# Optimization experiments

Hardware: AMD Instinct MI355X
Metric: run time of the kernel (lower is better)

## Reference

```python
import jax, jax.numpy as jnp
import numpy as np

WS = 8        # window size
NH = 8        # num heads


def setup_inputs() -> dict:
    key = jax.random.key(0)
    ks = jax.random.split(key, 6)
    B, C, H, W = 8, 256, 64, 64
    Cr = C // 4
    s = lambda n: 1.0 / np.sqrt(n)
    return {
        "x": jax.random.normal(ks[0], (B, C, H, W), jnp.float32),
        "ca_w1": jax.random.normal(ks[1], (Cr, C), jnp.float32) * s(C),
        "ca_b1": jnp.zeros((Cr,), jnp.float32),
        "ca_w2": jax.random.normal(ks[2], (C, Cr), jnp.float32) * s(Cr),
        "ca_b2": jnp.zeros((C,), jnp.float32),
        "in_proj_w": jax.random.normal(ks[3], (3 * C, C), jnp.float32) * s(C),
        "in_proj_b": jnp.zeros((3 * C,), jnp.float32),
        "out_proj_w": jax.random.normal(ks[4], (C, C), jnp.float32) * s(C),
        "out_proj_b": jnp.zeros((C,), jnp.float32),
    }


def reference(x, ca_w1, ca_b1, ca_w2, ca_b2, in_proj_w, in_proj_b, out_proj_w, out_proj_b):
    B, C, H, W = x.shape
    # ---- channel SE gate: AdaptiveAvgPool2d(1) -> 1x1 conv == linear ----
    pooled = x.mean(axis=(2, 3))                                   # [B, C]
    h1 = jax.nn.relu(pooled @ ca_w1.T + ca_b1)                     # [B, C/4]
    ca = jax.nn.sigmoid(h1 @ ca_w2.T + ca_b2)                      # [B, C]
    x = x * ca[:, :, None, None]

    # ---- window partition (non-overlapping unfold) ----
    Hw, Ww = H // WS, W // WS
    nwin = Hw * Ww
    xw = x.reshape(B, C, Hw, WS, Ww, WS).transpose(0, 1, 2, 4, 3, 5)   # [B,C,Hw,Ww,ws,ws]
    # view(B,C,nwin,ws*ws).permute(2,0,3,1).reshape(nwin*B, ws*ws, C)
    xw = xw.reshape(B, C, nwin, WS * WS).transpose(2, 0, 3, 1).reshape(nwin * B, WS * WS, C)

    # ---- nn.MultiheadAttention with batch_first=False: (L, N, E) ----
    # L = nwin*B (sequence!), N = ws*ws (batch!), E = C  -- faithful to source quirk
    L, N, _ = xw.shape
    hd = C // NH
    qkv = xw @ in_proj_w.T + in_proj_b                             # [L, N, 3C]
    q, k, v = jnp.split(qkv, 3, axis=-1)
    to_heads = lambda t: t.reshape(L, N, NH, hd).transpose(1, 2, 0, 3)  # [N, NH, L, hd]
    q, k, v = to_heads(q), to_heads(k), to_heads(v)
    scale = 1.0 / jnp.sqrt(jnp.asarray(hd, x.dtype))
    attn = jax.nn.softmax(jnp.einsum("nhld,nhmd->nhlm", q * scale, k), axis=-1)
    o = jnp.einsum("nhlm,nhmd->nhld", attn, v)                     # [N, NH, L, hd]
    o = o.transpose(2, 0, 1, 3).reshape(L, N, C)
    o = o @ out_proj_w.T + out_proj_b                              # [L, N, C]

    # ---- reshape back; nearest interpolate H*W -> H*W is identity ----
    o = o.reshape(nwin, B, WS * WS, C).transpose(1, 3, 0, 2)       # [B, C, nwin, ws*ws]
    x_out = o.reshape(B, C, H, W)
    return x + x_out
```

## Files before the change

kernel.cpp:

```cpp
#include <hip/hip_runtime.h>
#include <hip/hip_bf16.h>
#include <math.h>


typedef unsigned short ushort_t;
typedef unsigned int uint_t;
typedef __attribute__((ext_vector_type(8))) short bf16x8;
typedef __attribute__((ext_vector_type(4))) float f32x4;

#define ALPHA 0.25503486f

__device__ __forceinline__ uint_t pk_rne(float a, float b) {
    __hip_bfloat16 ha = __float2bfloat16(a), hb = __float2bfloat16(b);
    ushort_t ua = *(ushort_t*)&ha, ub = *(ushort_t*)&hb;
    return (uint_t)ua | ((uint_t)ub << 16);
}

__device__ __forceinline__ uint_t pk2(float a, float b) {
    union { float f; uint_t u; } ua, ub; ua.f = a; ub.f = b;
    return __builtin_amdgcn_perm(ua.u, ub.u, 0x03020706u);
}

__device__ __forceinline__ void gl_lds16(const ushort_t* g, ushort_t* l) {
    __builtin_amdgcn_global_load_lds(
        (__attribute__((address_space(1))) unsigned int*)(g),
        (__attribute__((address_space(3))) unsigned int*)(l), 16, 0, 0);
}

__global__ __launch_bounds__(256) void k_pre(const float* __restrict__ x,
                                             float* __restrict__ pooled,
                                             const float* __restrict__ ipw,
                                             ushort_t* __restrict__ Wqb,
                                             const float* __restrict__ opw,
                                             ushort_t* __restrict__ Wob) {
    int bx = blockIdx.x;
    int t = threadIdx.x;
    if (bx < 2048) {
        const float4* row4 = (const float4*)(x + (size_t)bx * 4096);
        float s = 0.f;
        for (int i = t; i < 1024; i += 256) {
            float4 v = row4[i];
            s += v.x + v.y + v.z + v.w;
        }
        __shared__ float red[256];
        red[t] = s;
        __syncthreads();
        for (int o = 128; o > 0; o >>= 1) {
            if (t < o) red[t] += red[t + o];
            __syncthreads();
        }
        if (t == 0) pooled[bx] = red[0] * (1.f / 4096.f);
    } else if (bx < 2144) {
        int i = (bx - 2048) * 256 + t;
        float sc = (i < 8192) ? ALPHA : 1.f;
        const float4* s4 = (const float4*)ipw + (size_t)i * 2;
        float4 a = s4[0], b = s4[1];
        uint4 u;
        u.x = pk_rne(a.x * sc, a.y * sc); u.y = pk_rne(a.z * sc, a.w * sc);
        u.z = pk_rne(b.x * sc, b.y * sc); u.w = pk_rne(b.z * sc, b.w * sc);
        *(uint4*)(Wqb + (size_t)i * 8) = u;
    } else {
        int i = (bx - 2144) * 256 + t;
        const float4* s4 = (const float4*)opw + (size_t)i * 2;
        float4 a = s4[0], b = s4[1];
        uint4 u;
        u.x = pk_rne(a.x, a.y); u.y = pk_rne(a.z, a.w);
        u.z = pk_rne(b.x, b.y); u.w = pk_rne(b.z, b.w);
        *(uint4*)(Wob + (size_t)i * 8) = u;
    }
}

__global__ __launch_bounds__(256) void k_cvt(const float* __restrict__ src,
                                             ushort_t* __restrict__ dst, int n8,
                                             int scale_n8, float scale) {
    int i = blockIdx.x * 256 + threadIdx.x;
    if (i >= n8) return;
    float sc = (i < scale_n8) ? scale : 1.f;
    const float4* s = (const float4*)src + (size_t)i * 2;
    float4 a = s[0], b = s[1];
    uint4 u;
    u.x = pk_rne(a.x * sc, a.y * sc); u.y = pk_rne(a.z * sc, a.w * sc);
    u.z = pk_rne(b.x * sc, b.y * sc); u.w = pk_rne(b.z * sc, b.w * sc);
    *(uint4*)(dst + (size_t)i * 8) = u;
}

__global__ __launch_bounds__(256) void k_se(const float* __restrict__ pooled,
                                            const float* __restrict__ w1,
                                            const float* __restrict__ b1,
                                            const float* __restrict__ w2,
                                            const float* __restrict__ b2,
                                            float* __restrict__ ca) {
    __shared__ float sp[2048];
    __shared__ float sh1[512];
    int t = threadIdx.x;
    for (int i = t; i < 2048; i += 256) sp[i] = pooled[i];
    __syncthreads();
    for (int o = t; o < 512; o += 256) {
        int b = o >> 6, m = o & 63;
        float s = b1[m];
        const float* wr = w1 + (size_t)m * 256;
        const float* pr = sp + b * 256;
        for (int c = 0; c < 256; c++) s += pr[c] * wr[c];
        sh1[o] = s > 0.f ? s : 0.f;
    }
    __syncthreads();
    for (int o = t; o < 2048; o += 256) {
        int b = o >> 8, m = o & 255;
        float s = b2[m];
        const float* wr = w2 + (size_t)m * 64;
        const float* hr = sh1 + b * 64;
        for (int c = 0; c < 64; c++) s += hr[c] * wr[c];
        ca[o] = 1.f / (1.f + __expf(-s));
    }
}

#define GPAD 524
__global__ __launch_bounds__(256) void k_gate(const float* __restrict__ x,
                                              const float* __restrict__ ca,
                                              ushort_t* __restrict__ Ab) {
    __shared__ __align__(16) ushort_t Ls[32 * GPAD];
    __shared__ float sca[32];
    int bx = blockIdx.x;
    int b = bx >> 6, hw = (bx >> 3) & 7, c0 = (bx & 7) * 32;
    int t = threadIdx.x;
    if (t < 32) sca[t] = ca[b * 256 + c0 + t];
    __syncthreads();
    const float4* xb = (const float4*)(x + ((size_t)(b * 256 + c0) * 64 + hw * 8) * 64);
#pragma unroll
    for (int i = 0; i < 16; i++) {
        int f = i * 256 + t;
        int ch = f >> 7, rem = f & 127, r = rem >> 4, w4 = rem & 15;
        float4 v = xb[(size_t)ch * 1024 + r * 16 + w4];
        float g = sca[ch];
        uint2 u;
        u.x = pk_rne(v.x * g, v.y * g);
        u.y = pk_rne(v.z * g, v.w * g);
        *(uint2*)&Ls[ch * GPAD + r * 64 + w4 * 4] = u;
    }
    __syncthreads();
#pragma unroll
    for (int i = 0; i < 8; i++) {
        int q = i * 256 + t;
        int rr = q >> 2, part = q & 3;
        int ww = rr >> 6, p = rr & 63;
        int px = (p >> 3) * 64 + ww * 8 + (p & 7);
        const ushort_t* ls = &Ls[part * 8 * GPAD + px];
        uint4 u;
        u.x = (uint_t)ls[0]        | ((uint_t)ls[GPAD] << 16);
        u.y = (uint_t)ls[2 * GPAD] | ((uint_t)ls[3 * GPAD] << 16);
        u.z = (uint_t)ls[4 * GPAD] | ((uint_t)ls[5 * GPAD] << 16);
        u.w = (uint_t)ls[6 * GPAD] | ((uint_t)ls[7 * GPAD] << 16);
        size_t m = (size_t)(((hw * 8 + ww) * 8 + b) * 64 + p);
        *(uint4*)(Ab + m * 256 + c0 + part * 8) = u;
    }
}

__global__ __launch_bounds__(256, 2) void k_gemm_qkv3(const ushort_t* __restrict__ A,
                                                      const ushort_t* __restrict__ Bw,
                                                      const float* __restrict__ bias,
                                                      ushort_t* __restrict__ Qb,
                                                      ushort_t* __restrict__ Kb,
                                                      ushort_t* __restrict__ Vb) {
    __shared__ __align__(16) ushort_t As[8192];
    __shared__ __align__(16) ushort_t Bs[16384];
    int tid = threadIdx.x;
    int lane = tid & 63, wave = tid >> 6;
    int wm = wave >> 1, wn = wave & 1;
    int col = lane & 15, quad = lane >> 4;
    int orig = blockIdx.x;
    int xcd = orig & 7;
    int i96 = orig >> 3;
    int mi = i96 / 3;
    int sec = i96 - mi * 3;
    int m0 = (xcd * 32 + mi) * 128;
    const ushort_t* Bsec = Bw + ((size_t)sec << 16);

    int cbase = wave * 64 + lane;
    const ushort_t* asrc[4];
    const ushort_t* bsrc[8];
#pragma unroll
    for (int q = 0; q < 4; q++) {
        int c = q * 256 + cbase;
        int row = c >> 3;
        int kp = (c & 7) ^ (row & 7);
        asrc[q] = A + (size_t)(m0 + row) * 256 + kp * 8;
    }
#pragma unroll
    for (int q = 0; q < 8; q++) {
        int c = q * 256 + cbase;
        int row = c >> 3;
        int kp = (c & 7) ^ (row & 7);
        bsrc[q] = Bsec + (size_t)row * 256 + kp * 8;
    }

    f32x4 acc[4][8];
#pragma unroll
    for (int i = 0; i < 4; i++)
#pragma unroll
        for (int j = 0; j < 8; j++) acc[i][j] = (f32x4){0.f, 0.f, 0.f, 0.f};

    for (int t = 0; t < 4; t++) {
        int k0 = t * 64;
#pragma unroll
        for (int q = 0; q < 4; q++) gl_lds16(asrc[q] + k0, &As[(q * 4 + wave) * 512]);
#pragma unroll
        for (int q = 0; q < 8; q++) gl_lds16(bsrc[q] + k0, &Bs[(q * 4 + wave) * 512]);
        __syncthreads();
#pragma unroll
        for (int kk = 0; kk < 2; kk++) {
            bf16x8 af[4], bfg[8];
#pragma unroll
            for (int i = 0; i < 4; i++) {
                int row = wm * 64 + i * 16 + col;
                af[i] = *(const bf16x8*)&As[row * 64 + ((kk * 4 + quad) ^ (row & 7)) * 8];
            }
#pragma unroll
            for (int j = 0; j < 8; j++) {
                int row = wn * 128 + j * 16 + col;
                bfg[j] = *(const bf16x8*)&Bs[row * 64 + ((kk * 4 + quad) ^ (row & 7)) * 8];
            }
#pragma unroll
            for (int i = 0; i < 4; i++)
#pragma unroll
                for (int j = 0; j < 8; j++)
                    acc[i][j] = __builtin_amdgcn_mfma_f32_16x16x32_bf16(bfg[j], af[i], acc[i][j], 0, 0, 0);
        }
        __syncthreads();
    }

    ushort_t* dst = (sec == 0) ? Qb : (sec == 1) ? Kb : Vb;
    float bsc = (sec == 0) ? ALPHA : 1.f;
    int nb0 = wn * 128 + quad * 4;
#pragma unroll
    for (int j = 0; j < 8; j++) {
        float4 bv = *(const float4*)(bias + sec * 256 + nb0 + j * 16);
        bv.x *= bsc; bv.y *= bsc; bv.z *= bsc; bv.w *= bsc;
#pragma unroll
        for (int i = 0; i < 4; i++) {
            int m = m0 + wm * 64 + i * 16 + col;
            uint2 st;
            st.x = pk_rne(acc[i][j][0] + bv.x, acc[i][j][1] + bv.y);
            st.y = pk_rne(acc[i][j][2] + bv.z, acc[i][j][3] + bv.w);
            *(uint2*)(dst + (size_t)m * 256 + nb0 + j * 16) = st;
        }
    }
}

__global__ __launch_bounds__(512, 4) void k_attn(const ushort_t* __restrict__ Qb,
                                                 const ushort_t* __restrict__ Kb,
                                                 const ushort_t* __restrict__ Vb,
                                                 ushort_t* __restrict__ AO) {
    __shared__ __align__(16) ushort_t Ks[512 * 32];
    __shared__ __align__(16) ushort_t Vt[32 * 512];
    int p = blockIdx.x >> 3, h = blockIdx.x & 7;
    int tid = threadIdx.x;
    int lane = tid & 63, wave = tid >> 6;
    int col = lane & 15, quad = lane >> 4;

#pragma unroll
    for (int it = 0; it < 4; it++) {
        int u = it * 512 + tid;
        int key = u >> 2, oct = u & 3;
        size_t grow = ((size_t)(key * 64 + p)) * 256 + h * 32 + oct * 8;
        int ck = oct ^ ((key >> 3) & 3);
        *(bf16x8*)&Ks[key * 32 + ck * 8] = *(const bf16x8*)(Kb + grow);
    }
#pragma unroll
    for (int it = 0; it < 2; it++) {
        int u = it * 512 + tid;
        int kp = u >> 2, oct = u & 3;
        int k0 = kp * 2;
        size_t g0 = ((size_t)(k0 * 64 + p)) * 256 + h * 32 + oct * 8;
        bf16x8 v0 = *(const bf16x8*)(Vb + g0);
        bf16x8 v1 = *(const bf16x8*)(Vb + g0 + 16384);
        int kc = kp >> 2;
#pragma unroll
        for (int j = 0; j < 8; j++) {
            int vc = oct * 8 + j;
            int kcs = kc ^ (vc & 7) ^ ((vc >> 3) << 1);
            uint_t pkv = (uint_t)(ushort_t)v0[j] | ((uint_t)(ushort_t)v1[j] << 16);
            *(uint_t*)&Vt[vc * 512 + kcs * 8 + (k0 & 7)] = pkv;
        }
    }

    bf16x8 qfrag[4];
#pragma unroll
    for (int i = 0; i < 4; i++) {
        int qt = wave * 4 + i;
        qfrag[i] = *(const bf16x8*)(Qb + ((size_t)((qt * 16 + col) * 64 + p)) * 256 + h * 32 + quad * 8);
    }

    f32x4 O0[4], O1[4];
    float qsum[4];
#pragma unroll
    for (int i = 0; i < 4; i++) {
        O0[i] = (f32x4){0.f, 0.f, 0.f, 0.f};
        O1[i] = (f32x4){0.f, 0.f, 0.f, 0.f};
        qsum[i] = 0.f;
    }
    const f32x4 zero = {0.f, 0.f, 0.f, 0.f};
    int R = col >> 2, r4 = lane & 3;
    int krow0 = 8 * R + r4;
    int vc0 = col, vc1 = col + 16;
    int sw0 = (vc0 & 7) ^ ((vc0 >> 3) << 1);
    int sw1 = (vc1 & 7) ^ ((vc1 >> 3) << 1);

    __syncthreads();

    for (int c = 0; c < 512; c += 32) {
        int row0 = c + krow0;
        int row1 = row0 + 4;
        int ckq = quad ^ ((row0 >> 3) & 3);
        bf16x8 kf0 = *(const bf16x8*)&Ks[row0 * 32 + ckq * 8];
        bf16x8 kf1 = *(const bf16x8*)&Ks[row1 * 32 + ckq * 8];
        int kc = (c >> 3) + quad;
        bf16x8 vf0 = *(const bf16x8*)&Vt[vc0 * 512 + ((kc ^ sw0) * 8)];
        bf16x8 vf1 = *(const bf16x8*)&Vt[vc1 * 512 + ((kc ^ sw1) * 8)];
#pragma unroll
        for (int i = 0; i < 4; i++) {
            f32x4 s0 = __builtin_amdgcn_mfma_f32_16x16x32_bf16(kf0, qfrag[i], zero, 0, 0, 0);
            f32x4 s1 = __builtin_amdgcn_mfma_f32_16x16x32_bf16(kf1, qfrag[i], zero, 0, 0, 0);
            float p0[4], p1[4];
#pragma unroll
            for (int r = 0; r < 4; r++) {
                p0[r] = __builtin_amdgcn_exp2f(s0[r]);
                p1[r] = __builtin_amdgcn_exp2f(s1[r]);
            }
            qsum[i] += ((p0[0] + p0[1]) + (p0[2] + p0[3])) + ((p1[0] + p1[1]) + (p1[2] + p1[3]));
            union { uint_t u[4]; bf16x8 v; } pb;
            pb.u[0] = pk2(p0[0], p0[1]);
            pb.u[1] = pk2(p0[2], p0[3]);
            pb.u[2] = pk2(p1[0], p1[1]);
            pb.u[3] = pk2(p1[2], p1[3]);
            O0[i] = __builtin_amdgcn_mfma_f32_16x16x32_bf16(vf0, pb.v, O0[i], 0, 0, 0);
            O1[i] = __builtin_amdgcn_mfma_f32_16x16x32_bf16(vf1, pb.v, O1[i], 0, 0, 0);
        }
    }

#pragma unroll
    for (int i = 0; i < 4; i++) {
        float s = qsum[i];
        s += __shfl_xor(s, 16);
        s += __shfl_xor(s, 32);
        float inv = 1.f / s;
        int qt = wave * 4 + i;
        ushort_t* dst = AO + ((size_t)((qt * 16 + col) * 64 + p)) * 256 + h * 32;
        uint2 st0, st1;
        st0.x = pk_rne(O0[i][0] * inv, O0[i][1] * inv);
        st0.y = pk_rne(O0[i][2] * inv, O0[i][3] * inv);
        st1.x = pk_rne(O1[i][0] * inv, O1[i][1] * inv);
        st1.y = pk_rne(O1[i][2] * inv, O1[i][3] * inv);
        *(uint2*)(dst + quad * 4) = st0;
        *(uint2*)(dst + 16 + quad * 4) = st1;
    }
}

__global__ __launch_bounds__(256, 2) void k_gemm_out2(const ushort_t* __restrict__ A,
                                                      const ushort_t* __restrict__ Bw,
                                                      const float* __restrict__ bias,
                                                      const float* __restrict__ x,
                                                      const float* __restrict__ ca,
                                                      float* __restrict__ out) {
    __shared__ __align__(16) ushort_t As[2][8192];
    __shared__ __align__(16) ushort_t Bs[2][8192];
    int tid = threadIdx.x;
    int lane = tid & 63, wave = tid >> 6;
    int wm = wave >> 1, wn = wave & 1;
    int col = lane & 15, quad = lane >> 4;
    int orig = blockIdx.x;
    int wgid = (orig & 7) * 64 + (orig >> 3);
    int n0 = (wgid & 1) * 128;
    int m0 = (wgid >> 1) * 128;
    int cbase = wave * 64 + lane;

    const ushort_t* asrc[4];
    const ushort_t* bsrc[4];
#pragma unroll
    for (int q = 0; q < 4; q++) {
        int c = q * 256 + cbase;
        int row = c >> 3;
        int kp = (c & 7) ^ (row & 7);
        asrc[q] = A + (size_t)(m0 + row) * 256 + kp * 8;
        bsrc[q] = Bw + (size_t)(n0 + row) * 256 + kp * 8;
    }

    f32x4 acc[4][4];
#pragma unroll
    for (int i = 0; i < 4; i++)
#pragma unroll
        for (int j = 0; j < 4; j++) acc[i][j] = (f32x4){0.f, 0.f, 0.f, 0.f};

#pragma unroll
    for (int q = 0; q < 4; q++) {
        gl_lds16(asrc[q], &As[0][(q * 4 + wave) * 512]);
        gl_lds16(bsrc[q], &Bs[0][(q * 4 + wave) * 512]);
    }
    __syncthreads();

#pragma unroll
    for (int t = 0; t < 4; t++) {
        if (t < 3) {
            int k0 = (t + 1) * 64;
            int nb = (t + 1) & 1;
#pragma unroll
            for (int q = 0; q < 4; q++) {
                gl_lds16(asrc[q] + k0, &As[nb][(q * 4 + wave) * 512]);
                gl_lds16(bsrc[q] + k0, &Bs[nb][(q * 4 + wave) * 512]);
            }
        }
        const ushort_t* Ac = As[t & 1];
        const ushort_t* Bc = Bs[t & 1];
#pragma unroll
        for (int kk = 0; kk < 2; kk++) {
            bf16x8 af[4], bfg[4];
#pragma unroll
            for (int i = 0; i < 4; i++) {
                int row = wm * 64 + i * 16 + col;
                af[i] = *(const bf16x8*)&Ac[row * 64 + ((kk * 4 + quad) ^ (row & 7)) * 8];
            }
#pragma unroll
            for (int j = 0; j < 4; j++) {
                int row = wn * 64 + j * 16 + col;
                bfg[j] = *(const bf16x8*)&Bc[row * 64 + ((kk * 4 + quad) ^ (row & 7)) * 8];
            }
#pragma unroll
            for (int i = 0; i < 4; i++)
#pragma unroll
                for (int j = 0; j < 4; j++)
                    acc[i][j] = __builtin_amdgcn_mfma_f32_16x16x32_bf16(bfg[j], af[i], acc[i][j], 0, 0, 0);
        }
        __syncthreads();
    }

    int lw = (m0 + wm * 64) >> 6;
    int b = lw & 7, w_idx = lw >> 3;
#pragma unroll
    for (int j = 0; j < 4; j++) {
        int nbase = n0 + wn * 64 + j * 16 + quad * 4;
        float4 bv = *(const float4*)(bias + nbase);
        float4 cv = *(const float4*)(ca + b * 256 + nbase);
#pragma unroll
        for (int i = 0; i < 4; i++) {
            int p = i * 16 + col;
#pragma unroll
            for (int r = 0; r < 4; r++) {
                int n = nbase + r;
                float bias_r = (r == 0) ? bv.x : (r == 1) ? bv.y : (r == 2) ? bv.z : bv.w;
                float ca_r = (r == 0) ? cv.x : (r == 1) ? cv.y : (r == 2) ? cv.z : cv.w;
                size_t oi = (((size_t)b * 256 + n) * 64 + w_idx) * 64 + p;
                out[oi] = acc[i][j][r] + bias_r + x[oi] * ca_r;
            }
        }
    }
}

extern "C" void kernel_launch(void* const* d_in, const int* in_sizes, int n_in,
                              void* d_out, int out_size, void* d_ws, size_t ws_size,
                              hipStream_t stream) {
    const float* x     = (const float*)d_in[0];
    const float* ca_w1 = (const float*)d_in[1];
    const float* ca_b1 = (const float*)d_in[2];
    const float* ca_w2 = (const float*)d_in[3];
    const float* ca_b2 = (const float*)d_in[4];
    const float* ipw   = (const float*)d_in[5];
    const float* ipb   = (const float*)d_in[6];
    const float* opw   = (const float*)d_in[7];
    const float* opb   = (const float*)d_in[8];
    float* out = (float*)d_out;

    char* ws = (char*)d_ws;
    const size_t MB16 = 16777216ull;
    ushort_t* Qb = (ushort_t*)(ws + 0);
    ushort_t* Kb = (ushort_t*)(ws + MB16);
    ushort_t* Vb = (ushort_t*)(ws + 2 * MB16);
    float* pooled = (float*)(ws + 3 * MB16);
    float* ca     = (float*)(ws + 3 * MB16 + 8192);

    ushort_t* Ab  = (ushort_t*)d_out;
    ushort_t* Wqb = (ushort_t*)((char*)d_out + MB16);

    const size_t WOB_OFF = 3 * MB16 + 16384;
    bool wob_early = (ws_size >= WOB_OFF + 131072);
    ushort_t* Wob = wob_early ? (ushort_t*)(ws + WOB_OFF) : Vb;

    k_pre<<<wob_early ? 2176 : 2144, 256, 0, stream>>>(x, pooled, ipw, Wqb, opw, Wob);
    k_se<<<1, 256, 0, stream>>>(pooled, ca_w1, ca_b1, ca_w2, ca_b2, ca);
    k_gate<<<512, 256, 0, stream>>>(x, ca, Ab);
    k_gemm_qkv3<<<768, 256, 0, stream>>>(Ab, Wqb, ipb, Qb, Kb, Vb);
    k_attn<<<512, 512, 0, stream>>>(Qb, Kb, Vb, Qb );
    if (!wob_early) k_cvt<<<32, 256, 0, stream>>>(opw, Vb, 8192, 0, 1.f);
    k_gemm_out2<<<512, 256, 0, stream>>>(Qb, Wob, opb, x, ca, out);
}
```

Measured before the change: 200.6 us.

## Shrink out-proj GEMM tile to 64x128 single-buffered, add MFMA priority hints in attention

The output-projection GEMM now uses 64-row M tiles with single-buffered LDS and twice as many blocks, and launch bounds allow four blocks per CU. The goal is higher occupancy and more parallelism in place of double buffering. Separately, the attention loop raises wave priority around its MFMA instructions via s_setprio so matrix work is issued ahead of other waves. The trade-off is losing load/compute overlap inside each GEMM block and reloading the weight tile more often.

```diff
diff --git a/kernel.cpp b/kernel.cpp
--- a/kernel.cpp
+++ b/kernel.cpp
@@ -318,8 +318,10 @@
         bf16x8 vf1 = *(const bf16x8*)&Vt[vc1 * 512 + ((kc ^ sw1) * 8)];
 #pragma unroll
         for (int i = 0; i < 4; i++) {
+            __builtin_amdgcn_s_setprio(1);
             f32x4 s0 = __builtin_amdgcn_mfma_f32_16x16x32_bf16(kf0, qfrag[i], zero, 0, 0, 0);
             f32x4 s1 = __builtin_amdgcn_mfma_f32_16x16x32_bf16(kf1, qfrag[i], zero, 0, 0, 0);
+            __builtin_amdgcn_s_setprio(0);
             float p0[4], p1[4];
 #pragma unroll
             for (int r = 0; r < 4; r++) {
@@ -332,8 +334,10 @@
             pb.u[1] = pk2(p0[2], p0[3]);
             pb.u[2] = pk2(p1[0], p1[1]);
             pb.u[3] = pk2(p1[2], p1[3]);
+            __builtin_amdgcn_s_setprio(1);
             O0[i] = __builtin_amdgcn_mfma_f32_16x16x32_bf16(vf0, pb.v, O0[i], 0, 0, 0);
             O1[i] = __builtin_amdgcn_mfma_f32_16x16x32_bf16(vf1, pb.v, O1[i], 0, 0, 0);
+            __builtin_amdgcn_s_setprio(0);
         }
     }
 
@@ -355,76 +359,72 @@
     }
 }
 
-__global__ __launch_bounds__(256, 2) void k_gemm_out2(const ushort_t* __restrict__ A,
+__global__ __launch_bounds__(256, 4) void k_gemm_out3(const ushort_t* __restrict__ A,
                                                       const ushort_t* __restrict__ Bw,
                                                       const float* __restrict__ bias,
                                                       const float* __restrict__ x,
                                                       const float* __restrict__ ca,
                                                       float* __restrict__ out) {
-    __shared__ __align__(16) ushort_t As[2][8192];
-    __shared__ __align__(16) ushort_t Bs[2][8192];
+    __shared__ __align__(16) ushort_t As[4096];
+    __shared__ __align__(16) ushort_t Bs[8192];
     int tid = threadIdx.x;
     int lane = tid & 63, wave = tid >> 6;
     int wm = wave >> 1, wn = wave & 1;
     int col = lane & 15, quad = lane >> 4;
     int orig = blockIdx.x;
-    int wgid = (orig & 7) * 64 + (orig >> 3);
-    int n0 = (wgid & 1) * 128;
-    int m0 = (wgid >> 1) * 128;
+    int xcd = orig & 7;
+    int i128 = orig >> 3;
+    int mi = i128 >> 1;
+    int ns = i128 & 1;
+    int m0 = (xcd * 64 + mi) * 64;
+    int n0 = ns * 128;
+
     int cbase = wave * 64 + lane;
-
-    const ushort_t* asrc[4];
+    const ushort_t* asrc[2];
     const ushort_t* bsrc[4];
+#pragma unroll
+    for (int q = 0; q < 2; q++) {
+        int c = q * 256 + cbase;
+        int row = c >> 3;
+        int kp = (c & 7) ^ (row & 7);
+        asrc[q] = A + (size_t)(m0 + row) * 256 + kp * 8;
+    }
 #pragma unroll
     for (int q = 0; q < 4; q++) {
         int c = q * 256 + cbase;
         int row = c >> 3;
         int kp = (c & 7) ^ (row & 7);
-        asrc[q] = A + (size_t)(m0 + row) * 256 + kp * 8;
         bsrc[q] = Bw + (size_t)(n0 + row) * 256 + kp * 8;
     }
 
-    f32x4 acc[4][4];
-#pragma unroll
-    for (int i = 0; i < 4; i++)
+    f32x4 acc[2][4];
+#pragma unroll
+    for (int i = 0; i < 2; i++)
 #pragma unroll
         for (int j = 0; j < 4; j++) acc[i][j] = (f32x4){0.f, 0.f, 0.f, 0.f};
 
-#pragma unroll
-    for (int q = 0; q < 4; q++) {
-        gl_lds16(asrc[q], &As[0][(q * 4 + wave) * 512]);
-        gl_lds16(bsrc[q], &Bs[0][(q * 4 + wave) * 512]);
-    }
-    __syncthreads();
-
-#pragma unroll
     for (int t = 0; t < 4; t++) {
-        if (t < 3) {
-            int k0 = (t + 1) * 64;
-            int nb = (t + 1) & 1;
-#pragma unroll
-            for (int q = 0; q < 4; q++) {
-                gl_lds16(asrc[q] + k0, &As[nb][(q * 4 + wave) * 512]);
-                gl_lds16(bsrc[q] + k0, &Bs[nb][(q * 4 + wave) * 512]);
-            }
-        }
-        const ushort_t* Ac = As[t & 1];
-        const ushort_t* Bc = Bs[t & 1];
+        int k0 = t * 64;
+#pragma unroll
+        for (int q = 0; q < 2; q++) gl_lds16(asrc[q] + k0, &As[(q * 4 + wave) * 512]);
+#pragma unroll
+        for (int q = 0; q < 4; q++) gl_lds16(bsrc[q] + k0, &Bs[(q * 4 + wave) * 512]);
+        __syncthreads();
 #pragma unroll
         for (int kk = 0; kk < 2; kk++) {
-            bf16x8 af[4], bfg[4];
-#pragma unroll
-            for (int i = 0; i < 4; i++) {
-                int row = wm * 64 + i * 16 + col;
-                af[i] = *(const bf16x8*)&Ac[row * 64 + ((kk * 4 + quad) ^ (row & 7)) * 8];
+            bf16x8 af[2], bfg[4];
+#pragma unroll
+            for (int i = 0; i < 2; i++) {
+                int row = wm * 32 + i * 16 + col;
+                af[i] = *(const bf16x8*)&As[row * 64 + ((kk * 4 + quad) ^ (row & 7)) * 8];
             }
 #pragma unroll
             for (int j = 0; j < 4; j++) {
                 int row = wn * 64 + j * 16 + col;
-                bfg[j] = *(const bf16x8*)&Bc[row * 64 + ((kk * 4 + quad) ^ (row & 7)) * 8];
-            }
-#pragma unroll
-            for (int i = 0; i < 4; i++)
+                bfg[j] = *(const bf16x8*)&Bs[row * 64 + ((kk * 4 + quad) ^ (row & 7)) * 8];
+            }
+#pragma unroll
+            for (int i = 0; i < 2; i++)
 #pragma unroll
                 for (int j = 0; j < 4; j++)
                     acc[i][j] = __builtin_amdgcn_mfma_f32_16x16x32_bf16(bfg[j], af[i], acc[i][j], 0, 0, 0);
@@ -432,7 +432,7 @@
         __syncthreads();
     }
 
-    int lw = (m0 + wm * 64) >> 6;
+    int lw = m0 >> 6;
     int b = lw & 7, w_idx = lw >> 3;
 #pragma unroll
     for (int j = 0; j < 4; j++) {
@@ -440,14 +440,14 @@
         float4 bv = *(const float4*)(bias + nbase);
         float4 cv = *(const float4*)(ca + b * 256 + nbase);
 #pragma unroll
-        for (int i = 0; i < 4; i++) {
-            int p = i * 16 + col;
+        for (int i = 0; i < 2; i++) {
+            int px = wm * 32 + i * 16 + col;
 #pragma unroll
             for (int r = 0; r < 4; r++) {
                 int n = nbase + r;
                 float bias_r = (r == 0) ? bv.x : (r == 1) ? bv.y : (r == 2) ? bv.z : bv.w;
                 float ca_r = (r == 0) ? cv.x : (r == 1) ? cv.y : (r == 2) ? cv.z : cv.w;
-                size_t oi = (((size_t)b * 256 + n) * 64 + w_idx) * 64 + p;
+                size_t oi = (((size_t)b * 256 + n) * 64 + w_idx) * 64 + px;
                 out[oi] = acc[i][j][r] + bias_r + x[oi] * ca_r;
             }
         }
@@ -489,5 +489,5 @@
     k_gemm_qkv3<<<768, 256, 0, stream>>>(Ab, Wqb, ipb, Qb, Kb, Vb);
     k_attn<<<512, 512, 0, stream>>>(Qb, Kb, Vb, Qb );
     if (!wob_early) k_cvt<<<32, 256, 0, stream>>>(opw, Vb, 8192, 0, 1.f);
-    k_gemm_out2<<<512, 256, 0, stream>>>(Qb, Wob, opb, x, ca, out);
-}
+    k_gemm_out3<<<1024, 256, 0, stream>>>(Qb, Wob, opb, x, ca, out);
+}
```

Measured after the change: 201.8 us. No clear change (+0.6%).
